# Performance work log

Measured on AMD Instinct MI355X. Metric: run time of the kernel, lower is better.

Reference implementation:

```python
import jax, jax.numpy as jnp
import numpy as np

N_HEAD = 16

def setup_inputs() -> dict:
    key = jax.random.key(0)
    ks = jax.random.split(key, 5)
    B, T, C = 4, 2048, 1024
    x = jax.random.normal(ks[0], (B, T, C), dtype=jnp.float32)
    # Linear params (torch nn.Linear: y = x @ W.T + b), init scaled like default
    s = 1.0 / np.sqrt(C)
    W_attn = jax.random.uniform(ks[1], (3 * C, C), dtype=jnp.float32, minval=-s, maxval=s)
    b_attn = jax.random.uniform(ks[2], (3 * C,), dtype=jnp.float32, minval=-s, maxval=s)
    W_proj = jax.random.uniform(ks[3], (C, C), dtype=jnp.float32, minval=-s, maxval=s)
    b_proj = jax.random.uniform(ks[4], (C,), dtype=jnp.float32, minval=-s, maxval=s)
    return {"x": x, "W_attn": W_attn, "b_attn": b_attn, "W_proj": W_proj, "b_proj": b_proj}

def reference(x, W_attn, b_attn, W_proj, b_proj):
    B, T, C = x.shape
    H = N_HEAD
    D = C // H
    qkv = jnp.einsum('btc,oc->bto', x, W_attn) + b_attn  # [B,T,3C]
    q, k, v = jnp.split(qkv, 3, axis=2)
    # [B,H,T,D]
    q = q.reshape(B, T, H, D).transpose(0, 2, 1, 3)
    k = k.reshape(B, T, H, D).transpose(0, 2, 1, 3)
    v = v.reshape(B, T, H, D).transpose(0, 2, 1, 3)
    att = jnp.einsum('bhtd,bhsd->bhts', q, k) * (1.0 / np.sqrt(D))  # [B,H,T,T]
    causal = jnp.tril(jnp.ones((T, T), dtype=bool))
    att = jnp.where(causal, att, -jnp.inf)
    att = jax.nn.softmax(att, axis=-1)
    y = jnp.einsum('bhts,bhsd->bhtd', att, v)  # [B,H,T,D]
    y = y.transpose(0, 2, 1, 3).reshape(B, T, C)
    return jnp.einsum('btc,oc->bto', y, W_proj) + b_proj
```

## Files before the change

### kernel.cpp

```cpp
#include <hip/hip_runtime.h>
#include <stdint.h>

typedef unsigned short u16;
typedef __attribute__((ext_vector_type(8))) short short8;
typedef __attribute__((ext_vector_type(4))) float float4v;

#define MFMA16(a, b, c) __builtin_amdgcn_mfma_f32_16x16x32_bf16((a), (b), (c), 0, 0, 0)

#define Q_SCALE 0.18033688011112042f

__device__ __forceinline__ int swz(int row, int col) {
  return row * 64 + (col & 7) + ((((col >> 3) ^ row) & 7) << 3);
}

__device__ __forceinline__ u16 f2b(float f) {
  union { float f; unsigned u; } x; x.f = f;
  unsigned r = x.u + 0x7fffu + ((x.u >> 16) & 1u);
  return (u16)(r >> 16);
}

__device__ __forceinline__ unsigned pack2(float a, float b) {
  return (unsigned)f2b(a) | ((unsigned)f2b(b) << 16);
}

__device__ __forceinline__ void load_lds_16(const void* g, void* l) {
  __builtin_amdgcn_global_load_lds((__attribute__((address_space(1))) void*)g,
                                   (__attribute__((address_space(3))) void*)l,
                                   16, 0, 0);
}

__global__ __launch_bounds__(256) void cvt_bf16(const float* __restrict__ in,
                                                u16* __restrict__ out, int n8) {
  int i = blockIdx.x * 256 + threadIdx.x;
  if (i >= n8) return;
  const float4* p = (const float4*)in + (size_t)i * 2;
  float4 a = p[0], b = p[1];
  uint4 w;
  w.x = pack2(a.x, a.y);
  w.y = pack2(a.z, a.w);
  w.z = pack2(b.x, b.y);
  w.w = pack2(b.z, b.w);
  *(uint4*)&out[(size_t)i * 8] = w;
}

__global__ __launch_bounds__(256) void transpose_v(const u16* __restrict__ V,
                                                   u16* __restrict__ Vt) {
  __shared__ u16 tile[64][72];
  const int bh = blockIdx.y;
  const int t0 = blockIdx.x * 64;
  const int tid = threadIdx.x;
  const int r = tid >> 3, c = (tid & 7) * 8;
#pragma unroll
  for (int h = 0; h < 2; ++h) {
    uint4 v = *(const uint4*)&V[((size_t)bh * 2048 + t0 + r + h * 32) * 64 + c];
    const u16* p = (const u16*)&v;
#pragma unroll
    for (int j = 0; j < 8; ++j) tile[c + j][r + h * 32] = p[j];
  }
  __syncthreads();
#pragma unroll
  for (int h = 0; h < 2; ++h) {
    uint4 w;
    u16* p = (u16*)&w;
#pragma unroll
    for (int j = 0; j < 8; ++j) p[j] = tile[r + h * 32][c + j];
    *(uint4*)&Vt[((size_t)bh * 64 + r + h * 32) * 2048 + t0 + c] = w;
  }
}

template <bool QKV_OUT>
__global__ __launch_bounds__(256) void gemm_bt(const u16* __restrict__ A,
                                               const u16* __restrict__ B,
                                               const float* __restrict__ bias,
                                               float* __restrict__ Cf,
                                               u16* __restrict__ QKV,
                                               int M, int N, int K) {
  __shared__ __align__(16) u16 As[128 * 64];
  __shared__ __align__(16) u16 Bs[128 * 64];
  const int tid = threadIdx.x;
  const int lane = tid & 63;
  const int wave = tid >> 6;
  const int quad = lane >> 4;
  const int l15 = lane & 15;
  const int bm0 = blockIdx.y * 128;
  const int bn0 = blockIdx.x * 128;
  const int wm = (wave & 1) * 64;
  const int wn = (wave >> 1) * 64;

  float4v acc[4][4];
#pragma unroll
  for (int i = 0; i < 4; ++i)
#pragma unroll
    for (int j = 0; j < 4; ++j) acc[i][j] = (float4v){0.f, 0.f, 0.f, 0.f};

  const int srow = wave * 32 + (lane >> 3);
  const int scol = ((lane & 7) ^ ((lane >> 3) & 7)) * 8;

  for (int k0 = 0; k0 < K; k0 += 64) {
#pragma unroll
    for (int s = 0; s < 4; ++s) {
      const int r = s * 8;
      load_lds_16(&A[(size_t)(bm0 + srow + r) * K + k0 + scol], &As[(wave * 32 + r) * 64]);
      load_lds_16(&B[(size_t)(bn0 + srow + r) * K + k0 + scol], &Bs[(wave * 32 + r) * 64]);
    }
    __builtin_amdgcn_s_waitcnt(0);
    __syncthreads();
#pragma unroll
    for (int ks = 0; ks < 2; ++ks) {
      short8 af[4], bf[4];
#pragma unroll
      for (int t = 0; t < 4; ++t) {
        af[t] = *(const short8*)&As[swz(wm + t * 16 + l15, ks * 32 + quad * 8)];
        bf[t] = *(const short8*)&Bs[swz(wn + t * 16 + l15, ks * 32 + quad * 8)];
      }
#pragma unroll
      for (int mt = 0; mt < 4; ++mt)
#pragma unroll
        for (int nt = 0; nt < 4; ++nt)
          acc[mt][nt] = MFMA16(af[mt], bf[nt], acc[mt][nt]);
    }
    __syncthreads();
  }

#pragma unroll
  for (int mt = 0; mt < 4; ++mt) {
    const int row0 = bm0 + wm + mt * 16 + quad * 4;
#pragma unroll
    for (int nt = 0; nt < 4; ++nt) {
      const int col = bn0 + wn + nt * 16 + l15;
      const float bs = bias[col];
      if constexpr (QKV_OUT) {
        const int which = col >> 10;
        const int rem = col & 1023;
        const int h = rem >> 6;
        const int d = rem & 63;
        const float sc = (which == 0) ? Q_SCALE : 1.0f;
#pragma unroll
        for (int i = 0; i < 4; ++i) {
          const int t = row0 + i;
          const int b = t >> 11;
          const int tt = t & 2047;
          QKV[(size_t)which * 8388608 +
              ((size_t)(b * 16 + h) * 2048 + tt) * 64 + d] = f2b((acc[mt][nt][i] + bs) * sc);
        }
      } else {
#pragma unroll
        for (int i = 0; i < 4; ++i)
          Cf[(size_t)(row0 + i) * N + col] = acc[mt][nt][i] + bs;
      }
    }
  }
}

__global__ __launch_bounds__(256) void attn_kernel(const u16* __restrict__ QKV,
                                                   const u16* __restrict__ Vt_g,
                                                   u16* __restrict__ Y) {
  const int bx = blockIdx.x;
  const int bh = blockIdx.y;
  const int b = bh >> 4, h = bh & 15;
  const int tid = threadIdx.x;
  const int lane = tid & 63;
  const int wave = tid >> 6;
  const int quad = lane >> 4;
  const int l15 = lane & 15;
  const int qt[2] = {bx, 31 - bx};

  const u16* Qg = QKV + (size_t)bh * 2048 * 64;
  const u16* Kg = QKV + 8388608 + (size_t)bh * 2048 * 64;
  const u16* Vg = Vt_g + (size_t)bh * 64 * 2048;

  __shared__ __align__(16) u16 Ks[3][64 * 64];
  __shared__ __align__(16) u16 Vt[3][64 * 64];

  short8 qf[2][2];
#pragma unroll
  for (int u = 0; u < 2; ++u)
#pragma unroll
    for (int ks = 0; ks < 2; ++ks)
      qf[u][ks] = *(const short8*)&Qg[(size_t)(qt[u] * 64 + wave * 16 + l15) * 64 + ks * 32 + quad * 8];

  float4v o[2][4];
  float rs[2] = {0.f, 0.f};
#pragma unroll
  for (int u = 0; u < 2; ++u)
#pragma unroll
    for (int i = 0; i < 4; ++i) o[u][i] = (float4v){0.f, 0.f, 0.f, 0.f};

  const int r8 = lane >> 3;
  const int c8 = ((lane & 7) ^ r8) * 8;
  auto stage = [&](int st_, int bufi) {
    const int sb = st_ * 64;
#pragma unroll
    for (int p = 0; p < 2; ++p) {
      const int c = wave * 2 + p;
      load_lds_16(&Kg[(size_t)(sb + c * 8 + r8) * 64 + c8], &Ks[bufi][c * 512]);
      load_lds_16(&Vg[(size_t)(c * 8 + r8) * 2048 + sb + c8], &Vt[bufi][c * 512]);
    }
  };

  const int last = qt[1];
  stage(0, 0);
  stage(1, 1);
  asm volatile("s_waitcnt vmcnt(4)" ::: "memory");
  __builtin_amdgcn_s_barrier();

  int cur = 0;
  for (int st = 0; st <= last; ++st) {
    const bool pf = (st + 2 <= last);
    if (pf) {
      int nb = cur + 2; if (nb >= 3) nb -= 3;
      stage(st + 2, nb);
    }
    const bool both = (st <= qt[0]);

    float4v s[2][4];
#pragma unroll
    for (int u = 0; u < 2; ++u)
#pragma unroll
      for (int nt = 0; nt < 4; ++nt) s[u][nt] = (float4v){0.f, 0.f, 0.f, 0.f};
    __builtin_amdgcn_s_setprio(1);
#pragma unroll
    for (int ks = 0; ks < 2; ++ks)
#pragma unroll
      for (int nt = 0; nt < 4; ++nt) {
        const short8 kf = *(const short8*)&Ks[cur][swz(nt * 16 + l15, ks * 32 + quad * 8)];
        s[1][nt] = MFMA16(kf, qf[1][ks], s[1][nt]);
        if (both) s[0][nt] = MFMA16(kf, qf[0][ks], s[0][nt]);
      }
    __builtin_amdgcn_s_setprio(0);

    short8 af[2][2];
#pragma unroll
    for (int u = 0; u < 2; ++u) {
      if (u == 0 && !both) continue;

      if (st == qt[u]) {
        const int qrow = wave * 16 + l15;
        const int kb = quad * 4;
#pragma unroll
        for (int nt = 0; nt < 4; ++nt)
#pragma unroll
          for (int i = 0; i < 4; ++i)
            if (kb + nt * 16 + i > qrow) s[u][nt][i] = -1e30f;
      }

      unsigned pkx[4], pky[4];
#pragma unroll
      for (int nt = 0; nt < 4; ++nt) {
        const float p0 = __builtin_amdgcn_exp2f(s[u][nt][0]);
        const float p1 = __builtin_amdgcn_exp2f(s[u][nt][1]);
        const float p2 = __builtin_amdgcn_exp2f(s[u][nt][2]);
        const float p3 = __builtin_amdgcn_exp2f(s[u][nt][3]);
        rs[u] += (p0 + p1) + (p2 + p3);
        pkx[nt] = pack2(p0, p1);
        pky[nt] = pack2(p2, p3);
      }

#pragma unroll
      for (int ks = 0; ks < 2; ++ks) {
        unsigned ax = pkx[2 * ks], bx2 = pkx[2 * ks + 1];
        unsigned ay = pky[2 * ks], by2 = pky[2 * ks + 1];
        asm("v_permlane32_swap_b32 %0, %1" : "+v"(ax), "+v"(bx2));
        asm("v_permlane16_swap_b32 %0, %1" : "+v"(ax), "+v"(bx2));
        asm("v_permlane32_swap_b32 %0, %1" : "+v"(ay), "+v"(by2));
        asm("v_permlane16_swap_b32 %0, %1" : "+v"(ay), "+v"(by2));
        uint4 w;
        w.x = ax; w.y = ay; w.z = bx2; w.w = by2;
        af[u][ks] = *(const short8*)&w;
      }
    }

    __builtin_amdgcn_s_setprio(1);
#pragma unroll
    for (int ks = 0; ks < 2; ++ks)
#pragma unroll
      for (int dt = 0; dt < 4; ++dt) {
        const short8 vf = *(const short8*)&Vt[cur][swz(dt * 16 + l15, ks * 32 + quad * 8)];
        o[1][dt] = MFMA16(af[1][ks], vf, o[1][dt]);
        if (both) o[0][dt] = MFMA16(af[0][ks], vf, o[0][dt]);
      }
    __builtin_amdgcn_s_setprio(0);

    if (pf) asm volatile("s_waitcnt vmcnt(4)" ::: "memory");
    else    asm volatile("s_waitcnt vmcnt(0)" ::: "memory");
    __builtin_amdgcn_s_barrier();

    ++cur; if (cur >= 3) cur = 0;
  }

#pragma unroll
  for (int u = 0; u < 2; ++u) {
    float r = rs[u];
    r += __shfl_xor(r, 16);
    r += __shfl_xor(r, 32);
    float linv[4];
#pragma unroll
    for (int i = 0; i < 4; ++i) linv[i] = 1.0f / __shfl(r, quad * 4 + i);
#pragma unroll
    for (int dt = 0; dt < 4; ++dt)
#pragma unroll
      for (int i = 0; i < 4; ++i) {
        const float v = o[u][dt][i] * linv[i];
        const int t = qt[u] * 64 + wave * 16 + quad * 4 + i;
        Y[((size_t)b * 2048 + t) * 1024 + h * 64 + dt * 16 + l15] = f2b(v);
      }
  }
}

extern "C" void kernel_launch(void* const* d_in, const int* in_sizes, int n_in,
                              void* d_out, int out_size, void* d_ws, size_t ws_size,
                              hipStream_t stream) {
  const float* x  = (const float*)d_in[0];
  const float* Wa = (const float*)d_in[1];
  const float* ba = (const float*)d_in[2];
  const float* Wp = (const float*)d_in[3];
  const float* bp = (const float*)d_in[4];
  float* out = (float*)d_out;

  u16* xb  = (u16*)d_ws;
  u16* Wab = xb + 8388608;
  u16* Wpb = Wab + 3145728;
  u16* qkv = Wpb + 1048576;
  u16* y   = xb;
  u16* vt  = (u16*)d_out;

  cvt_bf16<<<4096, 256, 0, stream>>>(x, xb, 1048576);
  cvt_bf16<<<1536, 256, 0, stream>>>(Wa, Wab, 393216);
  cvt_bf16<<<512, 256, 0, stream>>>(Wp, Wpb, 131072);

  gemm_bt<true><<<dim3(24, 64), 256, 0, stream>>>(xb, Wab, ba, nullptr, qkv, 8192, 3072, 1024);
  transpose_v<<<dim3(32, 64), 256, 0, stream>>>(qkv + 16777216, vt);
  attn_kernel<<<dim3(16, 64), 256, 0, stream>>>(qkv, vt, y);
  gemm_bt<false><<<dim3(8, 64), 256, 0, stream>>>(y, Wpb, bp, out, nullptr, 8192, 1024, 1024);
}
```

Baseline: 299.8 us.

## Load V fragments straight to registers and compute row sums via MFMA

Removes the LDS staging buffers for V^T. Each wave now loads its V fragments from global memory directly into registers, one tile ahead, and the vmcnt waits are reworked to match. The softmax row sums are computed with an extra MFMA against a ones vector instead of scalar adds and cross-lane shuffles. This cuts LDS traffic and footprint, which may raise occupancy. In exchange, every wave loads V redundantly from global or L2 and holds more registers, and row sums now come from bf16-rounded probabilities.

Result: slower. 331.7 us (+10.6%).

```diff
diff --git a/kernel.cpp b/kernel.cpp
--- a/kernel.cpp
+++ b/kernel.cpp
@@ -170,7 +170,6 @@
   const u16* Vg = Vt_g + (size_t)bh * 64 * 2048;
 
   __shared__ __align__(16) u16 Ks[3][64 * 64];
-  __shared__ __align__(16) u16 Vt[3][64 * 64];
 
   short8 qf[2][2];
 #pragma unroll
@@ -180,28 +179,43 @@
       qf[u][ks] = *(const short8*)&Qg[(size_t)(qt[u] * 64 + wave * 16 + l15) * 64 + ks * 32 + quad * 8];
 
   float4v o[2][4];
-  float rs[2] = {0.f, 0.f};
-#pragma unroll
-  for (int u = 0; u < 2; ++u)
+  float4v rsacc[2];
+#pragma unroll
+  for (int u = 0; u < 2; ++u) {
+    rsacc[u] = (float4v){0.f, 0.f, 0.f, 0.f};
 #pragma unroll
     for (int i = 0; i < 4; ++i) o[u][i] = (float4v){0.f, 0.f, 0.f, 0.f};
+  }
+
+  const short8 ones8 = {0x3F80, 0x3F80, 0x3F80, 0x3F80, 0x3F80, 0x3F80, 0x3F80, 0x3F80};
 
   const int r8 = lane >> 3;
   const int c8 = ((lane & 7) ^ r8) * 8;
-  auto stage = [&](int st_, int bufi) {
+  auto stageK = [&](int st_, int bufi) {
     const int sb = st_ * 64;
 #pragma unroll
     for (int p = 0; p < 2; ++p) {
       const int c = wave * 2 + p;
       load_lds_16(&Kg[(size_t)(sb + c * 8 + r8) * 64 + c8], &Ks[bufi][c * 512]);
-      load_lds_16(&Vg[(size_t)(c * 8 + r8) * 2048 + sb + c8], &Vt[bufi][c * 512]);
     }
   };
 
+  short8 vf[8];
+  auto load_vf = [&](int st_) {
+    const u16* VgS = Vg + st_ * 64;
+#pragma unroll
+    for (int ks = 0; ks < 2; ++ks)
+#pragma unroll
+      for (int dt = 0; dt < 4; ++dt)
+        vf[ks * 4 + dt] = *(const short8*)&VgS[(size_t)(dt * 16 + l15) * 2048 + ks * 32 + quad * 8];
+    asm volatile("" ::: "memory");
+  };
+
   const int last = qt[1];
-  stage(0, 0);
-  stage(1, 1);
-  asm volatile("s_waitcnt vmcnt(4)" ::: "memory");
+  stageK(0, 0);
+  stageK(1, 1);
+  load_vf(0);
+  asm volatile("s_waitcnt vmcnt(10)" ::: "memory");
   __builtin_amdgcn_s_barrier();
 
   int cur = 0;
@@ -209,7 +223,7 @@
     const bool pf = (st + 2 <= last);
     if (pf) {
       int nb = cur + 2; if (nb >= 3) nb -= 3;
-      stage(st + 2, nb);
+      stageK(st + 2, nb);
     }
     const bool both = (st <= qt[0]);
 
@@ -251,7 +265,6 @@
         const float p1 = __builtin_amdgcn_exp2f(s[u][nt][1]);
         const float p2 = __builtin_amdgcn_exp2f(s[u][nt][2]);
         const float p3 = __builtin_amdgcn_exp2f(s[u][nt][3]);
-        rs[u] += (p0 + p1) + (p2 + p3);
         pkx[nt] = pack2(p0, p1);
         pky[nt] = pack2(p2, p3);
       }
@@ -267,22 +280,24 @@
         uint4 w;
         w.x = ax; w.y = ay; w.z = bx2; w.w = by2;
         af[u][ks] = *(const short8*)&w;
-      }
-    }
+        rsacc[u] = MFMA16(af[u][ks], ones8, rsacc[u]);
+      }
+    }
+
+    if (pf) asm volatile("s_waitcnt vmcnt(2)" ::: "memory");
+    else    asm volatile("s_waitcnt vmcnt(0)" ::: "memory");
 
     __builtin_amdgcn_s_setprio(1);
 #pragma unroll
     for (int ks = 0; ks < 2; ++ks)
 #pragma unroll
       for (int dt = 0; dt < 4; ++dt) {
-        const short8 vf = *(const short8*)&Vt[cur][swz(dt * 16 + l15, ks * 32 + quad * 8)];
-        o[1][dt] = MFMA16(af[1][ks], vf, o[1][dt]);
-        if (both) o[0][dt] = MFMA16(af[0][ks], vf, o[0][dt]);
+        o[1][dt] = MFMA16(af[1][ks], vf[ks * 4 + dt], o[1][dt]);
+        if (both) o[0][dt] = MFMA16(af[0][ks], vf[ks * 4 + dt], o[0][dt]);
       }
     __builtin_amdgcn_s_setprio(0);
 
-    if (pf) asm volatile("s_waitcnt vmcnt(4)" ::: "memory");
-    else    asm volatile("s_waitcnt vmcnt(0)" ::: "memory");
+    if (st < last) load_vf(st + 1);
     __builtin_amdgcn_s_barrier();
 
     ++cur; if (cur >= 3) cur = 0;
@@ -290,12 +305,9 @@
 
 #pragma unroll
   for (int u = 0; u < 2; ++u) {
-    float r = rs[u];
-    r += __shfl_xor(r, 16);
-    r += __shfl_xor(r, 32);
     float linv[4];
 #pragma unroll
-    for (int i = 0; i < 4; ++i) linv[i] = 1.0f / __shfl(r, quad * 4 + i);
+    for (int i = 0; i < 4; ++i) linv[i] = 1.0f / rsacc[u][i];
 #pragma unroll
     for (int dt = 0; dt < 4; ++dt)
 #pragma unroll
```
